# Performance work log

Measured on AMD Instinct MI355X. Metric: run time of the kernel, lower is better.

Reference implementation:

```python
import jax, jax.numpy as jnp
import numpy as np

B, L, D = 256, 512, 768
ATTN_H, WIDTH_DIM = 1000, 20
BINS = jnp.array([1, 2, 3, 4, 5, 6, 7, 8, 12, 16, 20, 24, 32, 64, 128], dtype=jnp.int64)


def setup_inputs() -> dict:
    key = jax.random.key(0)
    ks = jax.random.split(key, 20)
    s = 0.02
    embeds = jax.random.normal(ks[0], (B, L, D), dtype=jnp.float32)
    spans = jnp.sort(jax.random.randint(ks[1], (B, 2), 0, L, dtype=jnp.int64), axis=1)
    inp = {
        "embeds": embeds,
        "spans": spans,
        # attention scorer: Linear(768,1000) -> LeakyReLU -> Linear(1000,1)
        "aw1": jax.random.normal(ks[2], (D, ATTN_H), dtype=jnp.float32) * s,
        "ab1": jnp.zeros((ATTN_H,), dtype=jnp.float32),
        "aw2": jax.random.normal(ks[3], (ATTN_H, 1), dtype=jnp.float32) * s,
        "ab2": jnp.zeros((1,), dtype=jnp.float32),
        # width embedding: [len(bins)+1 = 16, 20]
        "width_emb": jax.random.normal(ks[4], (16, WIDTH_DIM), dtype=jnp.float32) * s,
        # score MLP: 2324 -> 1024 -> 512 -> 256 -> 30
        "sw1": jax.random.normal(ks[5], (2324, 1024), dtype=jnp.float32) * s,
        "sb1": jnp.zeros((1024,), dtype=jnp.float32),
        "sw2": jax.random.normal(ks[6], (1024, 512), dtype=jnp.float32) * s,
        "sb2": jnp.zeros((512,), dtype=jnp.float32),
        "sw3": jax.random.normal(ks[7], (512, 256), dtype=jnp.float32) * s,
        "sb3": jnp.zeros((256,), dtype=jnp.float32),
        "sw4": jax.random.normal(ks[8], (256, 30), dtype=jnp.float32) * s,
        "sb4": jnp.zeros((30,), dtype=jnp.float32),
    }
    return inp


def reference(embeds, spans, aw1, ab1, aw2, ab2, width_emb,
              sw1, sb1, sw2, sb2, sw3, sb3, sw4, sb4):
    b, l, d = embeds.shape
    start, end = spans[:, 0], spans[:, 1]

    # gather start/end token embeds -> [B, 2*D]
    se = jnp.take_along_axis(embeds, spans[:, :, None], axis=1).reshape(b, 2 * d)

    # attention logits over all tokens: Linear -> LeakyReLU -> Linear
    h = jax.nn.leaky_relu(embeds @ aw1 + ab1)          # [B, L, 1000]
    attns = (h @ aw2 + ab2)[..., 0]                     # [B, L]

    # ragged per-span softmax pooling, vectorized via masking (inclusive span)
    cols = jnp.arange(l, dtype=spans.dtype)[None, :]
    mask = (cols >= start[:, None]) & (cols <= end[:, None])
    w = jax.nn.softmax(jnp.where(mask, attns, jnp.float32(-1e30)), axis=1)
    w = w * mask.astype(w.dtype)
    attn_embeds = jnp.einsum("bl,bld->bd", w, embeds)   # [B, D]

    # width bucket embedding
    widths = end - start + 1
    idx = jnp.sum(widths[:, None] > BINS[None, :], axis=1)
    wemb = width_emb[idx]                                # [B, 20]

    x = jnp.concatenate([se, attn_embeds, wemb], axis=1)  # [B, 2324]
    x = jax.nn.leaky_relu(x @ sw1 + sb1)
    x = jax.nn.leaky_relu(x @ sw2 + sb2)
    x = jax.nn.leaky_relu(x @ sw3 + sb3)
    return x @ sw4 + sb4                                  # [B, 30]
```

## Files before the change

### kernel.cpp

```cpp
#include <hip/hip_runtime.h>
#include <hip/hip_bf16.h>

#define B_   256
#define L_   512
#define D_   768
#define H_   1000
#define NPAD 1024
#define XDIM 2324
#define MAXPOS (B_*L_)

typedef _Float16 half8 __attribute__((ext_vector_type(8)));
typedef float    f32x4 __attribute__((ext_vector_type(4)));

__global__ __launch_bounds__(256) void scan_kernel(const int* __restrict__ spans,
                                                   int* __restrict__ meta) {
    int b = threadIdx.x;
    int s = spans[2 * b], e = spans[2 * b + 1];
    s = min(max(s, 0), L_ - 1);
    e = min(max(e, s), L_ - 1);
    int w = e - s + 1;
    __shared__ int sw[256];
    sw[b] = w;
    __syncthreads();
    for (int d = 1; d < 256; d <<= 1) {
        int v = 0;
        if (b >= d) v = sw[b - d];
        __syncthreads();
        if (b >= d) sw[b] += v;
        __syncthreads();
    }
    meta[b]       = sw[b] - w;
    meta[256 + b] = s;
    meta[512 + b] = e;
    if (b == 255) meta[768] = sw[255];
}

__global__ __launch_bounds__(256) void pos_fill(const int* __restrict__ meta,
                                                int* __restrict__ pos_list) {
    int b = blockIdx.x;
    int off = meta[b], start = meta[256 + b], end = meta[512 + b];
    int w = end - start + 1;
    for (int i = threadIdx.x; i < w; i += blockDim.x)
        pos_list[off + i] = (b << 16) | (start + i);
}

__global__ __launch_bounds__(256) void transpose_w(const float* __restrict__ aw1,
                                                   _Float16* __restrict__ WbT) {
    int k0 = blockIdx.x * 32, n0 = blockIdx.y * 32;
    int tx = threadIdx.x & 31, ty = threadIdx.x >> 5;
    __shared__ float T[32][33];
#pragma unroll
    for (int it = 0; it < 4; it++) {
        int k = k0 + ty + 8 * it;
        int n = n0 + tx;
        T[ty + 8 * it][tx] = (n < H_) ? aw1[(size_t)k * H_ + n] : 0.f;
    }
    __syncthreads();
#pragma unroll
    for (int it = 0; it < 4; it++) {
        int n = n0 + ty + 8 * it;
        WbT[(size_t)n * D_ + k0 + tx] = (_Float16)T[tx][ty + 8 * it];
    }
}

#define BM   128
#define BN   128
#define BKT  32
#define NKST (D_ / BKT)

#define GLD_LDS16(gsrc, ldst) \
    __builtin_amdgcn_global_load_lds((const __attribute__((address_space(1))) void*)(gsrc), \
                                     (__attribute__((address_space(3))) void*)(ldst), 16, 0, 0)

__global__ __launch_bounds__(256) void attn_gemm_v3(
    const float* __restrict__ embeds, const _Float16* __restrict__ WbT,
    const float* __restrict__ ab1, const float* __restrict__ aw2,
    const int* __restrict__ pos_list, const int* __restrict__ meta,
    float* __restrict__ attns) {
    int npos = meta[768];
    int m0 = blockIdx.x * BM;
    if (m0 >= npos) return;
    int n0 = blockIdx.y * BN;
    int t = threadIdx.x;
    int lane = t & 63, w = t >> 6;
    int q = lane >> 4, l15 = lane & 15;
    int wr = w >> 1, wc = w & 1;

    __shared__ alignas(16) _Float16 As[2][BM][BKT];
    __shared__ alignas(16) _Float16 Bs[2][BN * BKT];
    __shared__ unsigned rowoff[BM];

    if (t < BM) {
        unsigned off = 0;
        int m = m0 + t;
        if (m < npos) {
            int p = pos_list[m];
            off = (unsigned)((p >> 16) * (L_ * D_) + (p & 0xffff) * D_);
        }
        rowoff[t] = off;
    }
    __syncthreads();

    const int arow = t >> 1;
    const int acol = (t & 1) * 16;
    const float* aptr = embeds + rowoff[arow] + acol;

    const _Float16* bptr = WbT + (size_t)(n0 + (t >> 2)) * D_ + (t & 3) * 8;

    float4 ar0, ar1, ar2, ar3;
    auto loadA = [&](int k0) {
        const float* p = aptr + k0;
        ar0 = *(const float4*)(p + 0);
        ar1 = *(const float4*)(p + 4);
        ar2 = *(const float4*)(p + 8);
        ar3 = *(const float4*)(p + 12);
    };
    auto writeA = [&](int bbuf) {
        half8 h0, h1;
        h0[0] = (_Float16)ar0.x; h0[1] = (_Float16)ar0.y;
        h0[2] = (_Float16)ar0.z; h0[3] = (_Float16)ar0.w;
        h0[4] = (_Float16)ar1.x; h0[5] = (_Float16)ar1.y;
        h0[6] = (_Float16)ar1.z; h0[7] = (_Float16)ar1.w;
        h1[0] = (_Float16)ar2.x; h1[1] = (_Float16)ar2.y;
        h1[2] = (_Float16)ar2.z; h1[3] = (_Float16)ar2.w;
        h1[4] = (_Float16)ar3.x; h1[5] = (_Float16)ar3.y;
        h1[6] = (_Float16)ar3.z; h1[7] = (_Float16)ar3.w;
        *(half8*)&As[bbuf][arow][acol]     = h0;
        *(half8*)&As[bbuf][arow][acol + 8] = h1;
    };
    auto issueB = [&](int bbuf, int k0) {
        const _Float16* s0 = bptr + k0;
        _Float16* d0 = &Bs[bbuf][0] + w * 512;
        GLD_LDS16(s0, d0);
        const _Float16* s1 = s0 + (size_t)64 * D_;
        _Float16* d1 = d0 + 2048;
        GLD_LDS16(s1, d1);
    };

    f32x4 acc[4][4];
#pragma unroll
    for (int mi = 0; mi < 4; mi++)
#pragma unroll
        for (int ni = 0; ni < 4; ni++) acc[mi][ni] = (f32x4){0.f, 0.f, 0.f, 0.f};

    auto compute = [&](int bbuf) {
        half8 af[4], bf[4];
#pragma unroll
        for (int mi = 0; mi < 4; mi++)
            af[mi] = *(const half8*)&As[bbuf][wr * 64 + mi * 16 + l15][q * 8];
#pragma unroll
        for (int ni = 0; ni < 4; ni++)
            bf[ni] = *(const half8*)&Bs[bbuf][((wc * 64 + ni * 16 + l15) << 5) + q * 8];
#pragma unroll
        for (int mi = 0; mi < 4; mi++)
#pragma unroll
            for (int ni = 0; ni < 4; ni++)
                acc[mi][ni] = __builtin_amdgcn_mfma_f32_16x16x32_f16(
                    af[mi], bf[ni], acc[mi][ni], 0, 0, 0);
    };

    issueB(0, 0);
    loadA(0);
    writeA(0);
    __syncthreads();

    int buf = 0;
#pragma unroll 2
    for (int ks = 0; ks < NKST - 1; ks++) {
        int kn = (ks + 1) * BKT;
        issueB(buf ^ 1, kn);
        loadA(kn);
        compute(buf);
        writeA(buf ^ 1);
        __syncthreads();
        buf ^= 1;
    }
    compute(buf);

    int colb = n0 + wc * 64;
    float bj[4], aj[4];
#pragma unroll
    for (int ni = 0; ni < 4; ni++) {
        int col = colb + ni * 16 + l15;
        bool v = col < H_;
        bj[ni] = v ? ab1[col] : 0.f;
        aj[ni] = v ? aw2[col] : 0.f;
    }
#pragma unroll
    for (int mi = 0; mi < 4; mi++) {
#pragma unroll
        for (int r = 0; r < 4; r++) {
            float p = 0.f;
#pragma unroll
            for (int ni = 0; ni < 4; ni++) {
                float h = acc[mi][ni][r] + bj[ni];
                h = h > 0.f ? h : 0.01f * h;
                p += h * aj[ni];
            }
            p += __shfl_xor(p, 1);
            p += __shfl_xor(p, 2);
            p += __shfl_xor(p, 4);
            p += __shfl_xor(p, 8);
            if (l15 == 0) {
                int row = m0 + wr * 64 + mi * 16 + q * 4 + r;
                if (row < npos) atomicAdd(&attns[row], p);
            }
        }
    }
}

__global__ __launch_bounds__(256) void build_x(
    const float* __restrict__ embeds, const float* __restrict__ attns,
    const int* __restrict__ meta, const float* __restrict__ width_emb,
    float* __restrict__ x) {
    int b = blockIdx.x, s = blockIdx.y, t = threadIdx.x;
    int off = meta[b], start = meta[256 + b], end = meta[512 + b];
    int w = end - start + 1;
    __shared__ float sv[512];
    __shared__ float red[256];
    for (int i = t; i < w; i += 256) sv[i] = attns[off + i];
    __syncthreads();
    float m = -3.0e38f;
    for (int i = t; i < w; i += 256) m = fmaxf(m, sv[i]);
    red[t] = m;
    __syncthreads();
    for (int st = 128; st > 0; st >>= 1) {
        if (t < st) red[t] = fmaxf(red[t], red[t + st]);
        __syncthreads();
    }
    float mx = red[0];
    __syncthreads();
    float ssum = 0.f;
    for (int i = t; i < w; i += 256) {
        float e = __expf(sv[i] - mx);
        sv[i] = e;
        ssum += e;
    }
    red[t] = ssum;
    __syncthreads();
    for (int st = 128; st > 0; st >>= 1) {
        if (t < st) red[t] += red[t + st];
        __syncthreads();
    }
    float inv = 1.0f / red[0];
    __syncthreads();

    int dim = s * 256 + t;
    const float* base = embeds + ((size_t)b * L_ + start) * D_ + dim;
    float acc = 0.f;
    int i = 0;
    for (; i + 3 < w; i += 4) {
        float w0 = sv[i], w1 = sv[i + 1], w2 = sv[i + 2], w3 = sv[i + 3];
        const float* p = base + (size_t)i * D_;
        acc += w0 * p[0] + w1 * p[D_] + w2 * p[2 * D_] + w3 * p[3 * D_];
    }
    for (; i < w; i++) acc += sv[i] * base[(size_t)i * D_];

    float* xb = x + (size_t)b * XDIM;
    xb[1536 + dim] = acc * inv;
    xb[dim]        = base[0];
    xb[768 + dim]  = embeds[((size_t)b * L_ + end) * D_ + dim];
    if (s == 0 && t < 20) {
        const int bins[15] = {1, 2, 3, 4, 5, 6, 7, 8, 12, 16, 20, 24, 32, 64, 128};
        int idx = 0;
#pragma unroll
        for (int q2 = 0; q2 < 15; q2++) idx += (w > bins[q2]);
        xb[2304 + t] = width_emb[idx * 20 + t];
    }
}

__global__ __launch_bounds__(256) void mlp_gemm_sk(
    const float* __restrict__ A, const float* __restrict__ W,
    float* __restrict__ out, int M, int N, int K, int kchunk) {
    __shared__ float As[16][68];
    __shared__ float Ws[16][64];
    int t = threadIdx.x;
    int tx = t & 15, ty = t >> 4;
    int m0 = blockIdx.x * 64, n0 = blockIdx.y * 64;
    int ks = blockIdx.z * kchunk;
    int ke = min(ks + kchunk, K);
    if (ks >= ke) return;
    int ar = t >> 2, akc = (t & 3) * 4;
    int wk = t >> 4, wnc = (t & 15) * 4;
    bool n4 = ((N & 3) == 0);

    float acc[4][4];
#pragma unroll
    for (int i = 0; i < 4; i++)
#pragma unroll
        for (int j = 0; j < 4; j++) acc[i][j] = 0.f;

    auto loadA = [&](int k0) -> float4 {
        float4 r = make_float4(0.f, 0.f, 0.f, 0.f);
        int k = k0 + akc;
        if (k < ke) r = *(const float4*)(A + (size_t)(m0 + ar) * K + k);
        return r;
    };
    auto loadW = [&](int k0) -> float4 {
        float4 r = make_float4(0.f, 0.f, 0.f, 0.f);
        int k = k0 + wk;
        if (k < ke) {
            int n = n0 + wnc;
            const float* p = W + (size_t)k * N + n;
            if (n4) {
                r = *(const float4*)p;
            } else {
                float tmp[4];
#pragma unroll
                for (int q2 = 0; q2 < 4; q2++)
                    tmp[q2] = (n + q2 < N) ? p[q2] : 0.f;
                r = make_float4(tmp[0], tmp[1], tmp[2], tmp[3]);
            }
        }
        return r;
    };

    float4 aR = loadA(ks), wR = loadW(ks);
    for (int k0 = ks; k0 < ke; k0 += 16) {
        As[akc + 0][ar] = aR.x;
        As[akc + 1][ar] = aR.y;
        As[akc + 2][ar] = aR.z;
        As[akc + 3][ar] = aR.w;
        *(float4*)&Ws[wk][wnc] = wR;
        __syncthreads();
        if (k0 + 16 < ke) { aR = loadA(k0 + 16); wR = loadW(k0 + 16); }
#pragma unroll
        for (int kk = 0; kk < 16; kk++) {
            float4 a = *(const float4*)&As[kk][ty * 4];
            float4 b = *(const float4*)&Ws[kk][tx * 4];
            float av[4] = {a.x, a.y, a.z, a.w};
            float bv[4] = {b.x, b.y, b.z, b.w};
#pragma unroll
            for (int i = 0; i < 4; i++)
#pragma unroll
                for (int j = 0; j < 4; j++) acc[i][j] += av[i] * bv[j];
        }
        __syncthreads();
    }
#pragma unroll
    for (int i = 0; i < 4; i++) {
#pragma unroll
        for (int j = 0; j < 4; j++) {
            int nn = n0 + tx * 4 + j;
            if (nn < N)
                atomicAdd(&out[(size_t)(m0 + ty * 4 + i) * N + nn], acc[i][j]);
        }
    }
}

__global__ __launch_bounds__(256) void bias_act(
    const float* __restrict__ src, const float* __restrict__ bias,
    float* __restrict__ dst, int total, int N, int leaky) {
    int i = blockIdx.x * 256 + threadIdx.x;
    int stride = gridDim.x * 256;
    for (; i < total; i += stride) {
        float v = src[i] + bias[i % N];
        if (leaky) v = v > 0.f ? v : 0.01f * v;
        dst[i] = v;
    }
}

extern "C" void kernel_launch(void* const* d_in, const int* in_sizes, int n_in,
                              void* d_out, int out_size, void* d_ws, size_t ws_size,
                              hipStream_t stream) {
    const float* embeds    = (const float*)d_in[0];
    const int*   spans     = (const int*)d_in[1];
    const float* aw1       = (const float*)d_in[2];
    const float* ab1       = (const float*)d_in[3];
    const float* aw2       = (const float*)d_in[4];
    const float* width_emb = (const float*)d_in[6];
    const float* sw1 = (const float*)d_in[7],  *sb1 = (const float*)d_in[8];
    const float* sw2 = (const float*)d_in[9],  *sb2 = (const float*)d_in[10];
    const float* sw3 = (const float*)d_in[11], *sb3 = (const float*)d_in[12];
    const float* sw4 = (const float*)d_in[13], *sb4 = (const float*)d_in[14];
    float* out = (float*)d_out;

    char* ws = (char*)d_ws;
    float*     attns    = (float*)ws;
    int*       pos_list = (int*)(ws + (size_t)MAXPOS * 4);
    int*       meta     = (int*)(ws + (size_t)MAXPOS * 8);
    _Float16*  WbT      = (_Float16*)(ws + (size_t)MAXPOS * 8 + 4096);
    float* x  = (float*)(ws + (size_t)MAXPOS * 8 + 4096 + (size_t)NPAD * D_ * 2);
    float* y1 = x + (size_t)B_ * XDIM;
    float* y2 = y1 + (size_t)B_ * 1024;
    float* y3 = y2 + (size_t)B_ * 512;
    float* y4 = y3 + (size_t)B_ * 256;
    size_t ybytes = ((size_t)B_ * (1024 + 512 + 256 + 30)) * 4;

    hipMemsetAsync(y1, 0, ybytes, stream);
    hipMemsetAsync(attns, 0, (size_t)MAXPOS * 4, stream);
    scan_kernel<<<1, 256, 0, stream>>>(spans, meta);
    pos_fill<<<B_, 256, 0, stream>>>(meta, pos_list);
    transpose_w<<<dim3(D_ / 32, NPAD / 32), 256, 0, stream>>>(aw1, WbT);
    attn_gemm_v3<<<dim3(MAXPOS / BM, NPAD / BN), 256, 0, stream>>>(
        embeds, WbT, ab1, aw2, pos_list, meta, attns);
    build_x<<<dim3(B_, 3), 256, 0, stream>>>(embeds, attns, meta, width_emb, x);

    mlp_gemm_sk<<<dim3(4, 16, 8), 256, 0, stream>>>(x,  sw1, y1, B_, 1024, XDIM, 292);
    bias_act<<<256, 256, 0, stream>>>(y1, sb1, y1, B_ * 1024, 1024, 1);
    mlp_gemm_sk<<<dim3(4, 8, 8), 256, 0, stream>>>(y1, sw2, y2, B_, 512, 1024, 128);
    bias_act<<<128, 256, 0, stream>>>(y2, sb2, y2, B_ * 512, 512, 1);
    mlp_gemm_sk<<<dim3(4, 4, 8), 256, 0, stream>>>(y2, sw3, y3, B_, 256, 512, 64);
    bias_act<<<64, 256, 0, stream>>>(y3, sb3, y3, B_ * 256, 256, 1);
    mlp_gemm_sk<<<dim3(4, 1, 8), 256, 0, stream>>>(y3, sw4, y4, B_, 30, 256, 32);
    bias_act<<<30, 256, 0, stream>>>(y4, sb4, out, B_ * 30, 30, 0);
}
```

Measured before the change: 801.6 us.

## Widen attention GEMM tile to 256 columns and fuse bias-activation into MLP loads

The attention-score GEMM moves to 512-thread blocks with a 128x256 output tile, arranged as a 2x4 warp grid. The A tile (fp32 embeddings converted to fp16) is now shared across more N columns, so the embedding rows are gathered half as many times. Separately, the bias add and LeakyReLU of each MLP layer are folded into the next split-K GEMM's A-load, which removes three bias_act launches and their global round trips. The trade-offs are a larger shared-memory and register footprint per block, and bias and activation being recomputed redundantly across N-blocks.

After: 731.1 us. 8.8% less time.

```diff
diff --git a/kernel.cpp b/kernel.cpp
--- a/kernel.cpp
+++ b/kernel.cpp
@@ -64,7 +64,7 @@
 }
 
 #define BM   128
-#define BN   128
+#define BN   256
 #define BKT  32
 #define NKST (D_ / BKT)
 
@@ -72,7 +72,7 @@
     __builtin_amdgcn_global_load_lds((const __attribute__((address_space(1))) void*)(gsrc), \
                                      (__attribute__((address_space(3))) void*)(ldst), 16, 0, 0)
 
-__global__ __launch_bounds__(256) void attn_gemm_v3(
+__global__ __launch_bounds__(512, 4) void attn_gemm_v4(
     const float* __restrict__ embeds, const _Float16* __restrict__ WbT,
     const float* __restrict__ ab1, const float* __restrict__ aw2,
     const int* __restrict__ pos_list, const int* __restrict__ meta,
@@ -84,7 +84,7 @@
     int t = threadIdx.x;
     int lane = t & 63, w = t >> 6;
     int q = lane >> 4, l15 = lane & 15;
-    int wr = w >> 1, wc = w & 1;
+    int wr = w >> 2, wc = w & 3;
 
     __shared__ alignas(16) _Float16 As[2][BM][BKT];
     __shared__ alignas(16) _Float16 Bs[2][BN * BKT];
@@ -101,39 +101,32 @@
     }
     __syncthreads();
 
-    const int arow = t >> 1;
-    const int acol = (t & 1) * 16;
+    const int arow = t >> 2;
+    const int acol = (t & 3) * 8;
     const float* aptr = embeds + rowoff[arow] + acol;
 
     const _Float16* bptr = WbT + (size_t)(n0 + (t >> 2)) * D_ + (t & 3) * 8;
 
-    float4 ar0, ar1, ar2, ar3;
+    float4 ar0, ar1;
     auto loadA = [&](int k0) {
         const float* p = aptr + k0;
         ar0 = *(const float4*)(p + 0);
         ar1 = *(const float4*)(p + 4);
-        ar2 = *(const float4*)(p + 8);
-        ar3 = *(const float4*)(p + 12);
     };
     auto writeA = [&](int bbuf) {
-        half8 h0, h1;
+        half8 h0;
         h0[0] = (_Float16)ar0.x; h0[1] = (_Float16)ar0.y;
         h0[2] = (_Float16)ar0.z; h0[3] = (_Float16)ar0.w;
         h0[4] = (_Float16)ar1.x; h0[5] = (_Float16)ar1.y;
         h0[6] = (_Float16)ar1.z; h0[7] = (_Float16)ar1.w;
-        h1[0] = (_Float16)ar2.x; h1[1] = (_Float16)ar2.y;
-        h1[2] = (_Float16)ar2.z; h1[3] = (_Float16)ar2.w;
-        h1[4] = (_Float16)ar3.x; h1[5] = (_Float16)ar3.y;
-        h1[6] = (_Float16)ar3.z; h1[7] = (_Float16)ar3.w;
-        *(half8*)&As[bbuf][arow][acol]     = h0;
-        *(half8*)&As[bbuf][arow][acol + 8] = h1;
+        *(half8*)&As[bbuf][arow][acol] = h0;
     };
     auto issueB = [&](int bbuf, int k0) {
         const _Float16* s0 = bptr + k0;
         _Float16* d0 = &Bs[bbuf][0] + w * 512;
         GLD_LDS16(s0, d0);
-        const _Float16* s1 = s0 + (size_t)64 * D_;
-        _Float16* d1 = d0 + 2048;
+        const _Float16* s1 = s0 + (size_t)128 * D_;
+        _Float16* d1 = d0 + 4096;
         GLD_LDS16(s1, d1);
     };
 
@@ -270,8 +263,9 @@
 }
 
 __global__ __launch_bounds__(256) void mlp_gemm_sk(
-    const float* __restrict__ A, const float* __restrict__ W,
-    float* __restrict__ out, int M, int N, int K, int kchunk) {
+    const float* __restrict__ A, const float* __restrict__ abias, int aleaky,
+    const float* __restrict__ W, float* __restrict__ out,
+    int M, int N, int K, int kchunk) {
     __shared__ float As[16][68];
     __shared__ float Ws[16][64];
     int t = threadIdx.x;
@@ -293,7 +287,19 @@
     auto loadA = [&](int k0) -> float4 {
         float4 r = make_float4(0.f, 0.f, 0.f, 0.f);
         int k = k0 + akc;
-        if (k < ke) r = *(const float4*)(A + (size_t)(m0 + ar) * K + k);
+        if (k < ke) {
+            r = *(const float4*)(A + (size_t)(m0 + ar) * K + k);
+            if (abias) {
+                r.x += abias[k];     r.y += abias[k + 1];
+                r.z += abias[k + 2]; r.w += abias[k + 3];
+                if (aleaky) {
+                    r.x = r.x > 0.f ? r.x : 0.01f * r.x;
+                    r.y = r.y > 0.f ? r.y : 0.01f * r.y;
+                    r.z = r.z > 0.f ? r.z : 0.01f * r.z;
+                    r.w = r.w > 0.f ? r.w : 0.01f * r.w;
+                }
+            }
+        }
         return r;
     };
     auto loadW = [&](int k0) -> float4 {
@@ -392,16 +398,13 @@
     scan_kernel<<<1, 256, 0, stream>>>(spans, meta);
     pos_fill<<<B_, 256, 0, stream>>>(meta, pos_list);
     transpose_w<<<dim3(D_ / 32, NPAD / 32), 256, 0, stream>>>(aw1, WbT);
-    attn_gemm_v3<<<dim3(MAXPOS / BM, NPAD / BN), 256, 0, stream>>>(
+    attn_gemm_v4<<<dim3(MAXPOS / BM, NPAD / BN), 512, 0, stream>>>(
         embeds, WbT, ab1, aw2, pos_list, meta, attns);
     build_x<<<dim3(B_, 3), 256, 0, stream>>>(embeds, attns, meta, width_emb, x);
 
-    mlp_gemm_sk<<<dim3(4, 16, 8), 256, 0, stream>>>(x,  sw1, y1, B_, 1024, XDIM, 292);
-    bias_act<<<256, 256, 0, stream>>>(y1, sb1, y1, B_ * 1024, 1024, 1);
-    mlp_gemm_sk<<<dim3(4, 8, 8), 256, 0, stream>>>(y1, sw2, y2, B_, 512, 1024, 128);
-    bias_act<<<128, 256, 0, stream>>>(y2, sb2, y2, B_ * 512, 512, 1);
-    mlp_gemm_sk<<<dim3(4, 4, 8), 256, 0, stream>>>(y2, sw3, y3, B_, 256, 512, 64);
-    bias_act<<<64, 256, 0, stream>>>(y3, sb3, y3, B_ * 256, 256, 1);
-    mlp_gemm_sk<<<dim3(4, 1, 8), 256, 0, stream>>>(y3, sw4, y4, B_, 30, 256, 32);
+    mlp_gemm_sk<<<dim3(4, 16, 8), 256, 0, stream>>>(x,  nullptr, 0, sw1, y1, B_, 1024, XDIM, 292);
+    mlp_gemm_sk<<<dim3(4, 8, 8), 256, 0, stream>>>(y1, sb1, 1, sw2, y2, B_, 512, 1024, 128);
+    mlp_gemm_sk<<<dim3(4, 4, 8), 256, 0, stream>>>(y2, sb2, 1, sw3, y3, B_, 256, 512, 64);
+    mlp_gemm_sk<<<dim3(4, 1, 8), 256, 0, stream>>>(y3, sb3, 1, sw4, y4, B_, 30, 256, 32);
     bias_act<<<30, 256, 0, stream>>>(y4, sb4, out, B_ * 30, 30, 0);
 }
```
